# Performance work log

Measured on AMD Instinct MI355X. Metric: run time of the kernel, lower is better.

Reference implementation:

```python
import jax, jax.numpy as jnp
import numpy as np

N = 30000      # input points
M = 7500       # sampled queries = floor(N * ratio), ratio=0.25
K = 16         # neighbors per query
D_X = 64       # input feature dim
D_REL = 64     # point_pos_nn output dim
D_F = D_X + D_REL  # fij_hat dim = 128


def setup_inputs() -> dict:
    key = jax.random.key(0)
    ks = jax.random.split(key, 6)
    x = jax.random.normal(ks[0], (N, D_X), jnp.float32)
    pos = jax.random.normal(ks[1], (N, 3), jnp.float32)
    idx = jax.random.randint(ks[2], (M,), 0, N)
    W_pos = jax.random.normal(ks[3], (10, D_REL), jnp.float32) / jnp.sqrt(10.0)
    b_pos = jnp.zeros((D_REL,), jnp.float32)
    W_att = jax.random.normal(ks[4], (D_F, D_F), jnp.float32) / jnp.sqrt(float(D_F))
    b_att = jnp.zeros((D_F,), jnp.float32)
    W_glob = jax.random.normal(ks[5], (D_F, D_F), jnp.float32) / jnp.sqrt(float(D_F))
    b_glob = jnp.zeros((D_F,), jnp.float32)
    return {"x": x, "pos": pos, "idx": idx, "W_pos": W_pos, "b_pos": b_pos,
            "W_att": W_att, "b_att": b_att, "W_glob": W_glob, "b_glob": b_glob}


def reference(x, pos, idx, W_pos, b_pos, W_att, b_att, W_glob, b_glob):
    # --- KNN: brute-force squared distances from sampled queries to all points ---
    pos_q = pos[idx]                                         # [M, 3]
    d2 = ((pos_q * pos_q).sum(-1)[:, None]
          + (pos * pos).sum(-1)[None, :]
          - 2.0 * pos_q @ pos.T)                             # [M, N]
    _, nbr = jax.lax.top_k(-d2, K)                           # [M, K] neighbor indices

    # --- Local Spatial Encoding (message) ---
    pos_j = pos[nbr]                                         # [M, K, 3]
    pos_i = jnp.broadcast_to(pos_q[:, None, :], pos_j.shape) # [M, K, 3]
    vij = pos_i - pos_j                                      # [M, K, 3]
    dij = jnp.linalg.norm(vij, axis=-1, keepdims=True)       # [M, K, 1]
    rel = jnp.concatenate([pos_i, pos_j, vij, dij], axis=-1) # [M, K, 10]
    rij = jax.nn.relu(rel @ W_pos + b_pos)                   # [M, K, D_REL]

    # --- Attentive pooling ---
    fij = jnp.concatenate([x[nbr], rij], axis=-1)            # [M, K, D_F]
    g = fij @ W_att + b_att                                  # [M, K, D_F]
    s = jax.nn.softmax(g, axis=-1)                           # softmax over feature dim
    aggr = jnp.mean(s * fij, axis=1)                         # mean over K neighbors -> [M, D_F]

    # --- global_nn (update) ---
    return jax.nn.relu(aggr @ W_glob + b_glob)               # [M, D_F]
```

## Files before the change

### kernel.cpp

```cpp
#include <hip/hip_runtime.h>
#include <stdint.h>

#define KNB   16
#define GD    64
#define GTOT  (GD * GD * GD)
#define GORIG (-6.5f)
#define GEDGE 0.203125f
#define GINV  (1.0f / GEDGE)
#define CAPW  640

typedef short short8 __attribute__((ext_vector_type(8)));
typedef float floatx4 __attribute__((ext_vector_type(4)));

__device__ __forceinline__ unsigned short f2bf(float x) {
  union { float f; uint32_t u; } v; v.f = x;
  uint32_t u = v.u + 0x7FFFu + ((v.u >> 16) & 1u);
  return (unsigned short)(u >> 16);
}
__device__ __forceinline__ float bf2f(unsigned short b) {
  return __uint_as_float(((uint32_t)b) << 16);
}
__device__ __forceinline__ int cellco(float v) {
  int c = (int)floorf((v - GORIG) * GINV);
  return c < 0 ? 0 : (c > GD - 1 ? GD - 1 : c);
}

__global__ void zero_kernel(int* __restrict__ count) {
  int i = (blockIdx.x * 256 + threadIdx.x) * 4;
  *(int4*)(count + i) = make_int4(0, 0, 0, 0);
}

__global__ void prep_kernel(const float* __restrict__ x,
                            const float* __restrict__ pos,
                            const float* __restrict__ W_att,
                            unsigned short* __restrict__ xb,
                            float4* __restrict__ pos4,
                            unsigned short* __restrict__ Wt,
                            int* __restrict__ ptcell,
                            int* __restrict__ count, int N) {
  int id = blockIdx.x * 256 + threadIdx.x;
  int nx8 = N * 8;
  if (id < nx8) {
    const float4* src = (const float4*)x + (size_t)id * 2;
    float4 a = src[0], b = src[1];
    short8 v;
    v[0] = (short)f2bf(a.x); v[1] = (short)f2bf(a.y);
    v[2] = (short)f2bf(a.z); v[3] = (short)f2bf(a.w);
    v[4] = (short)f2bf(b.x); v[5] = (short)f2bf(b.y);
    v[6] = (short)f2bf(b.z); v[7] = (short)f2bf(b.w);
    *(short8*)(xb + (size_t)id * 8) = v;
  } else if (id < nx8 + N) {
    int j = id - nx8;
    float px = pos[3 * j], py = pos[3 * j + 1], pz = pos[3 * j + 2];
    float pp = fmaf(px, px, fmaf(py, py, pz * pz));
    pos4[j] = make_float4(px, py, pz, pp);
    int cid = (cellco(pz) * GD + cellco(py)) * GD + cellco(px);
    ptcell[j] = cid;
    atomicAdd(&count[cid], 1);
  } else if (id < nx8 + N + 128 * 128) {
    int t = id - nx8 - N;
    int c = t >> 7, f = t & 127;
    Wt[f * 128 + c] = f2bf(W_att[t]);
  }
}

__global__ __launch_bounds__(256) void scan1(const int* __restrict__ count,
                                             int* __restrict__ partial) {
  int b = blockIdx.x, t = threadIdx.x;
  int v = count[b * 256 + t];
#pragma unroll
  for (int off = 1; off < 64; off <<= 1) v += __shfl_xor(v, off);
  __shared__ int ws_[4];
  if ((t & 63) == 0) ws_[t >> 6] = v;
  __syncthreads();
  if (t == 0) partial[b] = ws_[0] + ws_[1] + ws_[2] + ws_[3];
}

__global__ __launch_bounds__(256) void scan2(int* __restrict__ partial,
                                             int* __restrict__ cell_start) {
  int t = threadIdx.x;
  int v0 = partial[t * 4], v1 = partial[t * 4 + 1];
  int v2 = partial[t * 4 + 2], v3 = partial[t * 4 + 3];
  int s1 = v0 + v1, s2 = s1 + v2, s3 = s2 + v3;
  int x = s3;
  int lane = t & 63, wv = t >> 6;
#pragma unroll
  for (int off = 1; off < 64; off <<= 1) {
    int y = __shfl_up(x, off);
    if (lane >= off) x += y;
  }
  __shared__ int wsum[4];
  if (lane == 63) wsum[wv] = x;
  __syncthreads();
  int base = 0;
  for (int k = 0; k < wv; ++k) base += wsum[k];
  int excl = base + x - s3;
  partial[t * 4]     = excl;
  partial[t * 4 + 1] = excl + v0;
  partial[t * 4 + 2] = excl + s1;
  partial[t * 4 + 3] = excl + s2;
  if (t == 255) cell_start[GTOT] = excl + s3;
}

__global__ __launch_bounds__(256) void scan3(const int* __restrict__ count,
                                             const int* __restrict__ partial,
                                             int* __restrict__ cell_start,
                                             int* __restrict__ cursor) {
  int b = blockIdx.x, t = threadIdx.x;
  int v = count[b * 256 + t];
  int x = v;
  int lane = t & 63, wv = t >> 6;
#pragma unroll
  for (int off = 1; off < 64; off <<= 1) {
    int y = __shfl_up(x, off);
    if (lane >= off) x += y;
  }
  __shared__ int wsum[4];
  if (lane == 63) wsum[wv] = x;
  __syncthreads();
  int base = partial[b];
  for (int k = 0; k < wv; ++k) base += wsum[k];
  int excl = base + x - v;
  cell_start[b * 256 + t] = excl;
  cursor[b * 256 + t] = excl;
}

__global__ void scatter_kernel(const float4* __restrict__ pos4,
                               const int* __restrict__ ptcell,
                               int* __restrict__ cursor,
                               float4* __restrict__ spos4,
                               int* __restrict__ sid, int N) {
  int j = blockIdx.x * 256 + threadIdx.x;
  if (j >= N) return;
  int cid = ptcell[j];
  int slot = atomicAdd(&cursor[cid], 1);
  spos4[slot] = pos4[j];
  sid[slot] = j;
}

__global__ __launch_bounds__(256) void knn_grid(
    const float4* __restrict__ pos4, const float4* __restrict__ spos4,
    const int* __restrict__ sid, const int* __restrict__ cell_start,
    const int* __restrict__ idx, int* __restrict__ nbr, int M) {
  __shared__ unsigned long long cand[4][CAPW];
  const int tid = threadIdx.x, wv = tid >> 6, ln = tid & 63;
  const int m = blockIdx.x * 4 + wv;
  if (m >= M) return;

  const float4 qp = pos4[idx[m]];
  const int cqx = cellco(qp.x), cqy = cellco(qp.y), cqz = cellco(qp.z);

  int tot = 0;
  unsigned long long taukey = ~0ull;
  bool done = false;
  for (int s = 1; s <= 64 && !done; ++s) {
    const int w = 2 * s + 1, npair = w * w;
    for (int base = 0; base < npair; base += 64) {
      int i = base + ln;
      int stA = 0, enA = 0, stB = 0, enB = 0;
      if (i < npair) {
        int dz = i / w - s, dy = i - (i / w) * w - s;
        int cz = cqz + dz, cy = cqy + dy;
        if (cz >= 0 && cz < GD && cy >= 0 && cy < GD) {
          int rowbase = (cz * GD + cy) * GD;
          int az = dz < 0 ? -dz : dz, ay = dy < 0 ? -dy : dy;
          int ch = az > ay ? az : ay;
          if (s == 1 || ch == s) {
            int x0 = cqx - s; if (x0 < 0) x0 = 0;
            int x1 = cqx + s; if (x1 > GD - 1) x1 = GD - 1;
            stA = cell_start[rowbase + x0];
            enA = cell_start[rowbase + x1 + 1];
          } else {
            int xl = cqx - s, xr = cqx + s;
            if (xl >= 0) {
              stA = cell_start[rowbase + xl];
              enA = cell_start[rowbase + xl + 1];
            }
            if (xr <= GD - 1) {
              stB = cell_start[rowbase + xr];
              enB = cell_start[rowbase + xr + 1];
            }
          }
        }
      }
#pragma unroll
      for (int part = 0; part < 2; ++part) {
        int st = part ? stB : stA, en = part ? enB : enA;
        unsigned long long mk = __ballot(en > st);
        while (mk) {
          int l = __ffsll((unsigned long long)mk) - 1;
          mk &= mk - 1;
          int stl = __shfl(st, l), enl = __shfl(en, l);
          for (int b2 = stl; b2 < enl; b2 += 64) {
            if (tot + 64 > CAPW) {
              unsigned long long c[CAPW / 64];
#pragma unroll
              for (int chk = 0; chk < CAPW / 64; ++chk) {
                int slot = chk * 64 + ln;
                c[chk] = (slot < tot) ? cand[wv][slot] : ~0ull;
              }
              unsigned long long last = 0;
#pragma unroll
              for (int r = 0; r < KNB; ++r) {
                unsigned long long mn = c[0];
#pragma unroll
                for (int chk = 1; chk < CAPW / 64; ++chk)
                  mn = (c[chk] < mn) ? c[chk] : mn;
#pragma unroll
                for (int off = 1; off < 64; off <<= 1) {
                  unsigned long long o = __shfl_xor(mn, off);
                  mn = (o < mn) ? o : mn;
                }
                if (ln == 0) cand[wv][r] = mn;
                last = mn;
#pragma unroll
                for (int chk = 0; chk < CAPW / 64; ++chk)
                  if (c[chk] == mn) c[chk] = ~0ull;
              }
              tot = KNB;
              taukey = last;
            }
            int p = b2 + ln;
            unsigned long long key = ~0ull;
            bool ok = false;
            if (p < enl) {
              float4 pj = spos4[p];
              float dot = fmaf(qp.x, pj.x, fmaf(qp.y, pj.y, qp.z * pj.z));
              float tt  = fmaf(-2.f, dot, pj.w);
              float d2  = fmaxf(qp.w + tt, 0.f);
              key = ((unsigned long long)__float_as_uint(d2) << 32) |
                    (uint32_t)sid[p];
              ok = key < taukey;
            }
            unsigned long long bm = __ballot(ok);
            int pos = __popcll(bm & ((1ull << ln) - 1ull));
            if (ok) cand[wv][tot + pos] = key;
            tot += __popcll(bm);
          }
        }
      }
    }
    if (tot >= KNB) {
      float fx = qp.x - GORIG, fy = qp.y - GORIG, fz = qp.z - GORIG;
      float r = 3.0e38f;
      if (cqx - s > 0)      r = fminf(r, fx - (float)(cqx - s) * GEDGE);
      if (cqx + s < GD - 1) r = fminf(r, (float)(cqx + s + 1) * GEDGE - fx);
      if (cqy - s > 0)      r = fminf(r, fy - (float)(cqy - s) * GEDGE);
      if (cqy + s < GD - 1) r = fminf(r, (float)(cqy + s + 1) * GEDGE - fy);
      if (cqz - s > 0)      r = fminf(r, fz - (float)(cqz - s) * GEDGE);
      if (cqz + s < GD - 1) r = fminf(r, (float)(cqz + s + 1) * GEDGE - fz);
      float r2 = (r > 1.0e19f) ? 3.0e38f : r * r;
      int cnt = 0;
      for (int chk = 0; chk * 64 < tot; ++chk) {
        int slot = chk * 64 + ln;
        unsigned long long key = cand[wv][slot];
        float d2v = __uint_as_float((uint32_t)(key >> 32));
        cnt += __popcll(__ballot(slot < tot && d2v <= r2));
      }
      if (cnt >= KNB) done = true;
    }
  }

  int nc = tot;
  unsigned long long c[CAPW / 64];
#pragma unroll
  for (int chk = 0; chk < CAPW / 64; ++chk) {
    int slot = chk * 64 + ln;
    unsigned long long k2 = cand[wv][slot];
    c[chk] = (slot < nc) ? k2 : ~0ull;
  }
#pragma unroll
  for (int r = 0; r < KNB; ++r) {
    unsigned long long mn = c[0];
#pragma unroll
    for (int chk = 1; chk < CAPW / 64; ++chk) mn = (c[chk] < mn) ? c[chk] : mn;
#pragma unroll
    for (int off = 1; off < 64; off <<= 1) {
      unsigned long long o = __shfl_xor(mn, off);
      mn = (o < mn) ? o : mn;
    }
    if (ln == 0) nbr[m * KNB + r] = (int)(uint32_t)mn;
#pragma unroll
    for (int chk = 0; chk < CAPW / 64; ++chk)
      if (c[chk] == mn) c[chk] = ~0ull;
  }
}

__global__ __launch_bounds__(256) void mid_kernel(
    const unsigned short* __restrict__ xb, const float4* __restrict__ pos4,
    const int* __restrict__ idx, const float* __restrict__ W_pos,
    const float* __restrict__ b_pos, const unsigned short* __restrict__ Wt,
    const float* __restrict__ b_att, const int* __restrict__ nbr,
    float* __restrict__ aggr, int M) {
  __shared__ __align__(16) unsigned short fijb[8][16][136];
  __shared__ int nbr_s[128];
  __shared__ float4 qpos_s[8];

  const int tid = threadIdx.x;
  const int wid = tid >> 6, lane = tid & 63;
  const int col = lane & 15, quad = lane >> 4;
  const int b = blockIdx.x;

  if (tid < 128) {
    int mq = b * 8 + (tid >> 4); if (mq >= M) mq = M - 1;
    nbr_s[tid] = nbr[mq * 16 + (tid & 15)];
  }
  if (tid < 8) {
    int mq = b * 8 + tid; if (mq >= M) mq = M - 1;
    qpos_s[tid] = pos4[idx[mq]];
  }
  float wp[10];
#pragma unroll
  for (int t = 0; t < 10; ++t) wp[t] = W_pos[t * 64 + lane];
  float bp = b_pos[lane];
  __syncthreads();

  {
    int rr = tid >> 1, h = tid & 1;
    int jn = nbr_s[rr];
    const short8* src = (const short8*)(xb + ((size_t)jn << 6) + (h << 5));
    short8 v0 = src[0], v1 = src[1], v2 = src[2], v3 = src[3];
    short8* dst = (short8*)&fijb[rr >> 4][rr & 15][h * 32];
    dst[0] = v0; dst[1] = v1; dst[2] = v2; dst[3] = v3;
  }
#pragma unroll
  for (int qi = 0; qi < 2; ++qi) {
    int q = wid * 2 + qi;
    float4 qp = qpos_s[q];
#pragma unroll 4
    for (int k = 0; k < 16; ++k) {
      int jn = nbr_s[q * 16 + k];
      float4 pj = pos4[jn];
      float vx = qp.x - pj.x, vy = qp.y - pj.y, vz = qp.z - pj.z;
      float dd = sqrtf(fmaf(vx, vx, fmaf(vy, vy, vz * vz)));
      float r = bp;
      r = fmaf(qp.x, wp[0], r); r = fmaf(qp.y, wp[1], r); r = fmaf(qp.z, wp[2], r);
      r = fmaf(pj.x, wp[3], r); r = fmaf(pj.y, wp[4], r); r = fmaf(pj.z, wp[5], r);
      r = fmaf(vx, wp[6], r);  r = fmaf(vy, wp[7], r);  r = fmaf(vz, wp[8], r);
      r = fmaf(dd, wp[9], r);
      r = fmaxf(r, 0.f);
      fijb[q][k][64 + lane] = f2bf(r);
    }
  }
  __syncthreads();

#pragma unroll 1
  for (int qi = 0; qi < 2; ++qi) {
    int q = wid * 2 + qi;
    int mq = b * 8 + q;

    short8 af[4];
#pragma unroll
    for (int cs = 0; cs < 4; ++cs)
      af[cs] = *(const short8*)&fijb[q][col][cs * 32 + quad * 8];

    floatx4 acc[8];
#pragma unroll
    for (int ft = 0; ft < 8; ++ft) {
      float bav = b_att[ft * 16 + col];
      floatx4 a = {bav, bav, bav, bav};
#pragma unroll
      for (int cs = 0; cs < 4; ++cs) {
        short8 bfrag =
            *(const short8*)&Wt[(ft * 16 + col) * 128 + cs * 32 + quad * 8];
        a = __builtin_amdgcn_mfma_f32_16x16x32_bf16(af[cs], bfrag, a, 0, 0, 0);
      }
      acc[ft] = a;
    }

    float rowmax[4], rowinv[4];
#pragma unroll
    for (int r = 0; r < 4; ++r) {
      float mx = acc[0][r];
#pragma unroll
      for (int ft = 1; ft < 8; ++ft) mx = fmaxf(mx, acc[ft][r]);
      mx = fmaxf(mx, __shfl_xor(mx, 1));
      mx = fmaxf(mx, __shfl_xor(mx, 2));
      mx = fmaxf(mx, __shfl_xor(mx, 4));
      mx = fmaxf(mx, __shfl_xor(mx, 8));
      float sm = 0.f;
#pragma unroll
      for (int ft = 0; ft < 8; ++ft) sm += __expf(acc[ft][r] - mx);
      sm += __shfl_xor(sm, 1);
      sm += __shfl_xor(sm, 2);
      sm += __shfl_xor(sm, 4);
      sm += __shfl_xor(sm, 8);
      rowmax[r] = mx;
      rowinv[r] = 1.0f / sm;
    }

#pragma unroll
    for (int ft = 0; ft < 8; ++ft) {
      float ap = 0.f;
#pragma unroll
      for (int r = 0; r < 4; ++r) {
        float s = __expf(acc[ft][r] - rowmax[r]) * rowinv[r];
        float fv = bf2f(fijb[q][quad * 4 + r][ft * 16 + col]);
        ap = fmaf(s, fv, ap);
      }
      ap += __shfl_xor(ap, 16);
      ap += __shfl_xor(ap, 32);
      if (quad == 0 && mq < M)
        aggr[mq * 128 + ft * 16 + col] = ap * (1.0f / 16.0f);
    }
  }
}

__global__ __launch_bounds__(256) void out_kernel(
    const float* __restrict__ aggr, const float* __restrict__ W_glob,
    const float* __restrict__ b_glob, float* __restrict__ out, int M) {
  __shared__ float ag[16][128];
  const int tid = threadIdx.x;
  const int mbase = blockIdx.x * 16;
  for (int s = tid; s < 16 * 128; s += 256) {
    int r = s >> 7, cc = s & 127;
    int m = mbase + r;
    ((float*)ag)[s] = (m < M) ? aggr[m * 128 + cc] : 0.0f;
  }
  __syncthreads();
  const int f = tid & 127, h = tid >> 7;
  float acc[8];
  float bg = b_glob[f];
#pragma unroll
  for (int i = 0; i < 8; ++i) acc[i] = bg;
  for (int c = 0; c < 128; c += 4) {
    float w0 = W_glob[(c + 0) * 128 + f];
    float w1 = W_glob[(c + 1) * 128 + f];
    float w2 = W_glob[(c + 2) * 128 + f];
    float w3 = W_glob[(c + 3) * 128 + f];
#pragma unroll
    for (int i = 0; i < 8; ++i) {
      const floatx4 a4 = *(const floatx4*)&ag[h * 8 + i][c];
      acc[i] += a4[0] * w0 + a4[1] * w1 + a4[2] * w2 + a4[3] * w3;
    }
  }
#pragma unroll
  for (int i = 0; i < 8; ++i) {
    int m = mbase + h * 8 + i;
    if (m < M) out[m * 128 + f] = fmaxf(acc[i], 0.0f);
  }
}

extern "C" void kernel_launch(void* const* d_in, const int* in_sizes, int n_in,
                              void* d_out, int out_size, void* d_ws,
                              size_t ws_size, hipStream_t stream) {
  const float* x      = (const float*)d_in[0];
  const float* pos    = (const float*)d_in[1];
  const int*   idx    = (const int*)d_in[2];
  const float* W_pos  = (const float*)d_in[3];
  const float* b_pos  = (const float*)d_in[4];
  const float* W_att  = (const float*)d_in[5];
  const float* b_att  = (const float*)d_in[6];
  const float* W_glob = (const float*)d_in[7];
  const float* b_glob = (const float*)d_in[8];
  float* out = (float*)d_out;

  const int N = in_sizes[1] / 3;
  const int M = in_sizes[2];

  char* ws = (char*)d_ws;
  size_t o = 0;
  float4* pos4 = (float4*)(ws + o);               o += ((size_t)N * 16 + 255) & ~(size_t)255;
  unsigned short* xb = (unsigned short*)(ws + o); o += ((size_t)N * 128 + 255) & ~(size_t)255;
  unsigned short* Wt = (unsigned short*)(ws + o); o += (128 * 128 * 2 + 255) & ~(size_t)255;
  int* nbr = (int*)(ws + o);                      o += (((size_t)M * KNB * 4) + 255) & ~(size_t)255;
  int* ptcell = (int*)(ws + o);                   o += (((size_t)N * 4) + 255) & ~(size_t)255;
  int* count = (int*)(ws + o);                    o += ((size_t)GTOT * 4 + 255) & ~(size_t)255;
  int* cursor = (int*)(ws + o);                   o += ((size_t)GTOT * 4 + 255) & ~(size_t)255;
  int* cell_start = (int*)(ws + o);               o += ((size_t)(GTOT + 1) * 4 + 255) & ~(size_t)255;
  int* partial = (int*)(ws + o);                  o += (1024 * 4 + 255) & ~(size_t)255;
  float4* spos4 = (float4*)(ws + o);              o += ((size_t)N * 16 + 255) & ~(size_t)255;
  int* sid = (int*)(ws + o);                      o += (((size_t)N * 4) + 255) & ~(size_t)255;
  float* aggr = (float*)(ws + o);                 o += ((size_t)M * 128 * 4 + 255) & ~(size_t)255;

  zero_kernel<<<GTOT / 1024, 256, 0, stream>>>(count);

  int prep_ids = N * 8 + N + 128 * 128;
  prep_kernel<<<(prep_ids + 255) / 256, 256, 0, stream>>>(
      x, pos, W_att, xb, pos4, Wt, ptcell, count, N);

  scan1<<<GTOT / 256, 256, 0, stream>>>(count, partial);
  scan2<<<1, 256, 0, stream>>>(partial, cell_start);
  scan3<<<GTOT / 256, 256, 0, stream>>>(count, partial, cell_start, cursor);

  scatter_kernel<<<(N + 255) / 256, 256, 0, stream>>>(pos4, ptcell, cursor,
                                                      spos4, sid, N);

  knn_grid<<<(M + 3) / 4, 256, 0, stream>>>(pos4, spos4, sid, cell_start, idx,
                                            nbr, M);

  mid_kernel<<<(M + 7) / 8, 256, 0, stream>>>(xb, pos4, idx, W_pos, b_pos, Wt,
                                              b_att, nbr, aggr, M);
  out_kernel<<<(M + 15) / 16, 256, 0, stream>>>(aggr, W_glob, b_glob, out, M);
}
```

Baseline: 212.0 us.

## Flatten KNN cell-range loops with wave prefix-sum and binary-search lane mapping

Replaces the per-lane serial walk over cell ranges (ballot, then iterate each lane's range in 64-wide chunks) with a wave-wide exclusive prefix sum over range lengths. Range descriptors are stored in LDS, and each lane finds its source range by binary search. Every 64-lane batch is then fully packed with candidate points, which removes the many partially filled iterations over small cells. The cost is a shuffle scan, LDS writes, and a 6-step LDS binary search per point.

```diff
diff --git a/kernel.cpp b/kernel.cpp
--- a/kernel.cpp
+++ b/kernel.cpp
@@ -143,6 +143,8 @@
     const int* __restrict__ sid, const int* __restrict__ cell_start,
     const int* __restrict__ idx, int* __restrict__ nbr, int M) {
   __shared__ unsigned long long cand[4][CAPW];
+  __shared__ uint32_t rsA[4][64], rlA[4][64], rsB[4][64];
+  __shared__ uint32_t rps[4][72];
   const int tid = threadIdx.x, wv = tid >> 6, ln = tid & 63;
   const int m = blockIdx.x * 4 + wv;
   if (m >= M) return;
@@ -157,7 +159,7 @@
     const int w = 2 * s + 1, npair = w * w;
     for (int base = 0; base < npair; base += 64) {
       int i = base + ln;
-      int stA = 0, enA = 0, stB = 0, enB = 0;
+      int stA = 0, lA = 0, stB = 0, lB = 0;
       if (i < npair) {
         int dz = i / w - s, dy = i - (i / w) * w - s;
         int cz = cqz + dz, cy = cqy + dy;
@@ -169,75 +171,90 @@
             int x0 = cqx - s; if (x0 < 0) x0 = 0;
             int x1 = cqx + s; if (x1 > GD - 1) x1 = GD - 1;
             stA = cell_start[rowbase + x0];
-            enA = cell_start[rowbase + x1 + 1];
+            lA  = cell_start[rowbase + x1 + 1] - stA;
           } else {
             int xl = cqx - s, xr = cqx + s;
             if (xl >= 0) {
               stA = cell_start[rowbase + xl];
-              enA = cell_start[rowbase + xl + 1];
+              lA  = cell_start[rowbase + xl + 1] - stA;
             }
             if (xr <= GD - 1) {
               stB = cell_start[rowbase + xr];
-              enB = cell_start[rowbase + xr + 1];
+              lB  = cell_start[rowbase + xr + 1] - stB;
             }
           }
         }
       }
-#pragma unroll
-      for (int part = 0; part < 2; ++part) {
-        int st = part ? stB : stA, en = part ? enB : enA;
-        unsigned long long mk = __ballot(en > st);
-        while (mk) {
-          int l = __ffsll((unsigned long long)mk) - 1;
-          mk &= mk - 1;
-          int stl = __shfl(st, l), enl = __shfl(en, l);
-          for (int b2 = stl; b2 < enl; b2 += 64) {
-            if (tot + 64 > CAPW) {
-              unsigned long long c[CAPW / 64];
-#pragma unroll
-              for (int chk = 0; chk < CAPW / 64; ++chk) {
-                int slot = chk * 64 + ln;
-                c[chk] = (slot < tot) ? cand[wv][slot] : ~0ull;
-              }
-              unsigned long long last = 0;
-#pragma unroll
-              for (int r = 0; r < KNB; ++r) {
-                unsigned long long mn = c[0];
-#pragma unroll
-                for (int chk = 1; chk < CAPW / 64; ++chk)
-                  mn = (c[chk] < mn) ? c[chk] : mn;
-#pragma unroll
-                for (int off = 1; off < 64; off <<= 1) {
-                  unsigned long long o = __shfl_xor(mn, off);
-                  mn = (o < mn) ? o : mn;
-                }
-                if (ln == 0) cand[wv][r] = mn;
-                last = mn;
-#pragma unroll
-                for (int chk = 0; chk < CAPW / 64; ++chk)
-                  if (c[chk] == mn) c[chk] = ~0ull;
-              }
-              tot = KNB;
-              taukey = last;
+      int len = lA + lB;
+      int xinc = len;
+#pragma unroll
+      for (int off = 1; off < 64; off <<= 1) {
+        int y = __shfl_up(xinc, off);
+        if (ln >= off) xinc += y;
+      }
+      int T = __shfl(xinc, 63);
+      if (T == 0) continue;
+      rps[wv][ln] = (uint32_t)(xinc - len);
+      if (ln == 63) rps[wv][64] = (uint32_t)T;
+      rsA[wv][ln] = (uint32_t)stA;
+      rlA[wv][ln] = (uint32_t)lA;
+      rsB[wv][ln] = (uint32_t)stB;
+
+      for (int b2 = 0; b2 < T; b2 += 64) {
+        if (tot + 64 > CAPW) {
+          unsigned long long c[CAPW / 64];
+#pragma unroll
+          for (int chk = 0; chk < CAPW / 64; ++chk) {
+            int slot = chk * 64 + ln;
+            c[chk] = (slot < tot) ? cand[wv][slot] : ~0ull;
+          }
+          unsigned long long last = 0;
+#pragma unroll
+          for (int r = 0; r < KNB; ++r) {
+            unsigned long long mn = c[0];
+#pragma unroll
+            for (int chk = 1; chk < CAPW / 64; ++chk)
+              mn = (c[chk] < mn) ? c[chk] : mn;
+#pragma unroll
+            for (int off = 1; off < 64; off <<= 1) {
+              unsigned long long o = __shfl_xor(mn, off);
+              mn = (o < mn) ? o : mn;
             }
-            int p = b2 + ln;
-            unsigned long long key = ~0ull;
-            bool ok = false;
-            if (p < enl) {
-              float4 pj = spos4[p];
-              float dot = fmaf(qp.x, pj.x, fmaf(qp.y, pj.y, qp.z * pj.z));
-              float tt  = fmaf(-2.f, dot, pj.w);
-              float d2  = fmaxf(qp.w + tt, 0.f);
-              key = ((unsigned long long)__float_as_uint(d2) << 32) |
-                    (uint32_t)sid[p];
-              ok = key < taukey;
-            }
-            unsigned long long bm = __ballot(ok);
-            int pos = __popcll(bm & ((1ull << ln) - 1ull));
-            if (ok) cand[wv][tot + pos] = key;
-            tot += __popcll(bm);
+            if (ln == 0) cand[wv][r] = mn;
+            last = mn;
+#pragma unroll
+            for (int chk = 0; chk < CAPW / 64; ++chk)
+              if (c[chk] == mn) c[chk] = ~0ull;
           }
+          tot = KNB;
+          taukey = last;
         }
+        int flat = b2 + ln;
+        unsigned long long key = ~0ull;
+        bool ok = false;
+        if (flat < T) {
+          int lo = 0;
+#pragma unroll
+          for (int step = 32; step > 0; step >>= 1) {
+            int mid = lo + step;
+            if (mid <= 63 && (int)rps[wv][mid] <= flat) lo = mid;
+          }
+          int o = flat - (int)rps[wv][lo];
+          uint32_t sa = rsA[wv][lo], la = rlA[wv][lo];
+          int p = (o < (int)la) ? (int)(sa + o)
+                                : (int)(rsB[wv][lo] + (uint32_t)(o - (int)la));
+          float4 pj = spos4[p];
+          float dot = fmaf(qp.x, pj.x, fmaf(qp.y, pj.y, qp.z * pj.z));
+          float tt  = fmaf(-2.f, dot, pj.w);
+          float d2  = fmaxf(qp.w + tt, 0.f);
+          key = ((unsigned long long)__float_as_uint(d2) << 32) |
+                (uint32_t)sid[p];
+          ok = key < taukey;
+        }
+        unsigned long long bm = __ballot(ok);
+        int pos = __popcll(bm & ((1ull << ln) - 1ull));
+        if (ok) cand[wv][tot + pos] = key;
+        tot += __popcll(bm);
       }
     }
     if (tot >= KNB) {
```

New measurement: 202.3 us. 1.05x faster.
